# Kernel optimization log

Measured on AMD Instinct MI355X. Metric: run time of the kernel, lower is better.

The kernel has to match this reference:

```python
import jax, jax.numpy as jnp
import numpy as np

N_NODES, D_IN, D_OUT, N_REL, N_EDGES = 100000, 128, 128, 8, 625000


def setup_inputs() -> dict:
    key = jax.random.key(0)
    ks = jax.random.split(key, 6)
    x = jax.random.normal(ks[0], (N_NODES, D_IN), dtype=jnp.float32)
    edge_index = jax.random.randint(ks[1], (2, N_EDGES), 0, N_NODES, dtype=jnp.int64)
    edge_type = jax.random.randint(ks[2], (N_EDGES,), 0, N_REL, dtype=jnp.int64)
    lim = (6.0 / (D_IN + D_OUT)) ** 0.5  # xavier_uniform
    rel_weight = jax.random.uniform(ks[3], (N_REL, D_IN, D_OUT), jnp.float32, -lim, lim)
    self_loop_weight = jax.random.uniform(ks[4], (D_IN, D_OUT), jnp.float32, -lim, lim)
    bias = jnp.zeros((D_OUT,), jnp.float32)
    return dict(x=x, edge_index=edge_index, edge_type=edge_type,
                rel_weight=rel_weight, self_loop_weight=self_loop_weight, bias=bias)


def reference(x, edge_index, edge_type, rel_weight, self_loop_weight, bias):
    N = x.shape[0]
    R = rel_weight.shape[0]
    src, dst = edge_index[0], edge_index[1]
    # Per-(relation, dst) in-degree == torch.bincount(dst) within each relation mask.
    seg = edge_type * N + dst  # combined (rel, dst) segment id
    deg = jax.ops.segment_sum(jnp.ones_like(src, dtype=x.dtype), seg, num_segments=R * N)
    deg = jnp.maximum(deg, 1.0)
    # Transform all node features by each relation weight once: [R, N, Do].
    xW = jnp.einsum('nd,rde->rne', x, rel_weight)
    # Gather per-edge messages already transformed by the edge's relation.
    messages = xW[edge_type, src] / deg[seg][:, None]  # [E, Do]
    out = x @ self_loop_weight + jax.ops.segment_sum(messages, dst, num_segments=N)
    return out + bias
```

## Files before the change

kernel.cpp:

```cpp
#include <hip/hip_runtime.h>

#define N_NODES 100000
#define DIM 128
#define N_REL 8
#define N_EDGES 625000
#define RN 800000
#define N_PADROWS 100032
#define SCAN_BLOCKS 98
#define SCAN_CHUNK 8192

__device__ __forceinline__ unsigned short f2bf(float f) {
    unsigned int u = __float_as_uint(f);
    u += 0x7fffu + ((u >> 16) & 1u);
    return (unsigned short)(u >> 16);
}

__device__ __forceinline__ float bf2f(unsigned short s) {
    return __uint_as_float(((unsigned int)s) << 16);
}

__global__ __launch_bounds__(256) void prep_kernel(const float* __restrict__ x,
                                                   const float* __restrict__ relw,
                                                   const float* __restrict__ selfw,
                                                   const int* __restrict__ dst,
                                                   const int* __restrict__ rel,
                                                   unsigned short* __restrict__ xb,
                                                   unsigned short* __restrict__ Wt,
                                                   int* __restrict__ degi,
                                                   int* __restrict__ rank) {
    int i = blockIdx.x * 256 + threadIdx.x;
    {
        float4 v = *(const float4*)(x + (size_t)i * 4);
        unsigned short t[4] = {f2bf(v.x), f2bf(v.y), f2bf(v.z), f2bf(v.w)};
        *(uint2*)(xb + (size_t)i * 4) = *(const uint2*)t;
    }
    if (i < 512) {
        uint4 z = {0, 0, 0, 0};
        *(uint4*)(xb + (size_t)N_NODES * DIM + i * 8) = z;
    }
    if (i < 147456) {
        int j = i & 7;
        int lane = (i >> 3) & 63;
        int t = (i >> 9) & 7;
        int ks = (i >> 12) & 3;
        int r = i >> 14;
        int m16 = lane & 15, quad = lane >> 4;
        int din = ks * 32 + quad * 8 + j;
        int dout = t * 16 + m16;
        float v = (r < 8) ? relw[(r << 14) + (din << 7) + dout] : selfw[(din << 7) + dout];
        Wt[i] = f2bf(v);
    }
    if (i < N_EDGES) {
        rank[i] = atomicAdd(&degi[rel[i] * N_NODES + dst[i]], 1);
    }
}

__global__ __launch_bounds__(256) void scan_kernel(const int* __restrict__ degi,
                                                   unsigned int* __restrict__ status,
                                                   int* __restrict__ offs) {
    __shared__ int lsum[256];
    __shared__ int lpfx;
    const int tid = threadIdx.x;
    const int b = blockIdx.x;
    const int base = b * SCAN_CHUNK + tid * 32;
    int v[32];
    int s = 0;
#pragma unroll
    for (int j = 0; j < 8; j++) {
        int idx = base + j * 4;
        int4 d = {0, 0, 0, 0};
        if (idx + 3 < RN) d = *(const int4*)(degi + idx);
        else {
            if (idx < RN) d.x = degi[idx];
            if (idx + 1 < RN) d.y = degi[idx + 1];
            if (idx + 2 < RN) d.z = degi[idx + 2];
        }
        v[j * 4] = d.x; v[j * 4 + 1] = d.y; v[j * 4 + 2] = d.z; v[j * 4 + 3] = d.w;
        s += d.x + d.y + d.z + d.w;
    }
    lsum[tid] = s;
    __syncthreads();
    for (int off = 1; off < 256; off <<= 1) {
        int p = (tid >= off) ? lsum[tid - off] : 0;
        __syncthreads();
        lsum[tid] += p;
        __syncthreads();
    }
    int thrbase = lsum[tid] - s;
    int total = lsum[255];

    if (b == 0) {
        if (tid == 0) {
            atomicExch(&status[0], 0x80000000u | (unsigned)total);
            lpfx = 0;
        }
    } else {
        if (tid == 0) atomicExch(&status[b], 0x40000000u | (unsigned)total);
        if (tid < 64) {
            int sum = 0;
            int j = b - 1;
            while (true) {
                int idx = j - tid;
                unsigned st = (idx >= 0) ? atomicAdd(&status[idx], 0u) : 0x80000000u;
                unsigned long long pball = __ballot(st & 0x80000000u);
                unsigned long long zball = __ballot(st == 0u);
                int fp = pball ? (__ffsll(pball) - 1) : 64;
                unsigned long long below = (fp >= 64) ? ~0ull : ((1ull << fp) - 1ull);
                if (zball & below) continue;
                int lim = (fp < 64) ? fp : 63;
                int val = (tid <= lim) ? (int)(st & 0x3fffffffu) : 0;
                for (int o = 32; o > 0; o >>= 1) val += __shfl_down(val, o);
                sum += __shfl(val, 0);
                if (fp < 64) break;
                j -= 64;
            }
            if (tid == 0) {
                atomicExch(&status[b], 0x80000000u | (unsigned)(sum + total));
                lpfx = sum;
            }
        }
    }
    __syncthreads();
    int run = lpfx + thrbase;
#pragma unroll
    for (int j = 0; j < 32; j++) {
        int idx = base + j;
        if (idx < RN) {
            offs[idx] = run;
            if (idx == RN - 1) offs[RN] = run + v[j];
            run += v[j];
        }
    }
}

__global__ __launch_bounds__(256) void fill_kernel(const int* __restrict__ src,
                                                   const int* __restrict__ dst,
                                                   const int* __restrict__ rel,
                                                   const int* __restrict__ rank,
                                                   const int* __restrict__ offs,
                                                   unsigned int* __restrict__ ebuf) {
    int e = blockIdx.x * 256 + threadIdx.x;
    if (e < N_EDGES) {
        int d = dst[e];
        int key = rel[e] * N_NODES + d;
        int pos = offs[key] + rank[e];
        ebuf[pos] = (unsigned int)src[e] | ((unsigned int)(d & 15) << 17);
    }
}

typedef __attribute__((ext_vector_type(8))) short frag8;
typedef __attribute__((ext_vector_type(4))) float f32x4;

__global__ __launch_bounds__(128, 5) void fused_kernel(const unsigned short* __restrict__ xb,
                                                       const unsigned short* __restrict__ Wt,
                                                       const int* __restrict__ offs2,
                                                       const unsigned int* __restrict__ ebuf,
                                                       const float* __restrict__ bias,
                                                       float* __restrict__ out) {
    __shared__ __align__(16) unsigned char ldsraw[8192];

    const int tid = threadIdx.x;
    const int h = tid >> 6, lane = tid & 63;
    const int m16 = lane & 15, quad = lane >> 4;
    const int dbase = blockIdx.x * 16;
    unsigned char* slab = ldsraw + h * 4096;

    int cidx = dbase + lane;
    if (cidx > N_NODES) cidx = N_NODES;
    const int* obase = offs2 + (size_t)h * 4 * N_NODES + cidx;

    int obc = obase[0];
    int obn = obase[N_NODES];

    f32x4 acc[8];
#pragma unroll
    for (int t = 0; t < 8; t++) acc[t] = (f32x4){0.f, 0.f, 0.f, 0.f};

    int s0 = __builtin_amdgcn_readlane(obc, 0);
    int count = __builtin_amdgcn_readlane(obc, 16) - s0;
    unsigned int ewc = 0;
    if (lane < count) ewc = ebuf[s0 + lane];

    {
        const unsigned short* ap = xb + (size_t)(dbase + m16) * DIM;
#pragma unroll
        for (int k2 = 0; k2 < 2; k2++) {
            int ks = h * 2 + k2;
            frag8 a = *(const frag8*)(ap + ks * 32 + quad * 8);
            const frag8* bp = (const frag8*)Wt + ((8 * 4 + ks) * 8) * 64 + lane;
#pragma unroll
            for (int t = 0; t < 8; t++)
                acc[t] = __builtin_amdgcn_mfma_f32_16x16x32_bf16(a, bp[t * 64], acc[t], 0, 0, 0);
        }
    }

    unsigned int u0[8], v0[8];
    if (count > 0) {
        int cl = count; if (cl > 64) cl = 64;
#pragma unroll
        for (int k = 0; k < 8; k++) {
            int li = k; if (li >= cl) li = cl - 1;
            u0[k] = (unsigned int)__builtin_amdgcn_readlane((int)ewc, li);
            v0[k] = *((const unsigned int*)xb + (size_t)(u0[k] & 0x1ffffu) * 64 + lane);
        }
    }

#pragma unroll 1
    for (int r = 0; r < 4; r++) {
        int s0n = __builtin_amdgcn_readlane(obn, 0);
        int cntn = __builtin_amdgcn_readlane(obn, 16) - s0n;
        unsigned int ewn = 0;
        if (r < 3 && lane < cntn) ewn = ebuf[s0n + lane];
        int obn2 = (r < 2) ? obase[(r + 2) * N_NODES] : 0;

        {
            uint4 z = {0, 0, 0, 0};
            *(uint4*)(slab + lane * 16) = z;
            *(uint4*)(slab + 1024 + lane * 16) = z;
            *(uint4*)(slab + 2048 + lane * 16) = z;
            *(uint4*)(slab + 3072 + lane * 16) = z;
        }

        if (count > 0) {
            float ax = 0.f, ay = 0.f;
            int cur = -1, cnt = 0;
#pragma unroll 1
            for (int b0 = 0; b0 < count; b0 += 64) {
                int cl = count - b0; if (cl > 64) cl = 64;
                unsigned int ew = ewc;
                if (b0 > 0) {
                    ew = 0;
                    if (b0 + lane < count) ew = ebuf[s0 + b0 + lane];
#pragma unroll
                    for (int k = 0; k < 8; k++) {
                        int li = k; if (li >= cl) li = cl - 1;
                        u0[k] = (unsigned int)__builtin_amdgcn_readlane((int)ew, li);
                        v0[k] = *((const unsigned int*)xb + (size_t)(u0[k] & 0x1ffffu) * 64 + lane);
                    }
                }
#pragma unroll 1
                for (int i = 0; i < cl; i += 8) {
                    unsigned int u1[8], v1[8];
                    if (i + 8 < cl) {
#pragma unroll
                        for (int k = 0; k < 8; k++) {
                            int li = i + 8 + k; if (li >= cl) li = cl - 1;
                            u1[k] = (unsigned int)__builtin_amdgcn_readlane((int)ew, li);
                            v1[k] = *((const unsigned int*)xb + (size_t)(u1[k] & 0x1ffffu) * 64 + lane);
                        }
                    }
                    int kk = cl - i; if (kk > 8) kk = 8;
#pragma unroll
                    for (int k = 0; k < 8; k++) {
                        if (k < kk) {
                            int dl = (int)((u0[k] >> 17) & 15u);
                            if (dl != cur) {
                                if (cnt > 0) {
                                    float inv = __builtin_amdgcn_rcpf((float)cnt);
                                    unsigned int p = (unsigned int)f2bf(ax * inv) |
                                                     ((unsigned int)f2bf(ay * inv) << 16);
                                    int bb = (lane >> 2) ^ cur;
                                    *(unsigned int*)(slab + cur * 256 + bb * 16 + (lane & 3) * 4) = p;
                                }
                                cur = dl; ax = 0.f; ay = 0.f; cnt = 0;
                            }
                            ax += bf2f((unsigned short)(v0[k] & 0xffffu));
                            ay += bf2f((unsigned short)(v0[k] >> 16));
                            cnt++;
                        }
                    }
                    if (i + 8 < cl) {
#pragma unroll
                        for (int k = 0; k < 8; k++) { u0[k] = u1[k]; v0[k] = v1[k]; }
                    }
                }
            }
            {
                float inv = __builtin_amdgcn_rcpf((float)cnt);
                unsigned int p = (unsigned int)f2bf(ax * inv) |
                                 ((unsigned int)f2bf(ay * inv) << 16);
                int bb = (lane >> 2) ^ cur;
                *(unsigned int*)(slab + cur * 256 + bb * 16 + (lane & 3) * 4) = p;
            }
        }

        if (r < 3 && cntn > 0) {
            int cl = cntn; if (cl > 64) cl = 64;
#pragma unroll
            for (int k = 0; k < 8; k++) {
                int li = k; if (li >= cl) li = cl - 1;
                u0[k] = (unsigned int)__builtin_amdgcn_readlane((int)ewn, li);
                v0[k] = *((const unsigned int*)xb + (size_t)(u0[k] & 0x1ffffu) * 64 + lane);
            }
        }

#pragma unroll
        for (int ks = 0; ks < 4; ks++) {
            int bb = (4 * ks + quad) ^ m16;
            frag8 a = *(const frag8*)(slab + m16 * 256 + bb * 16);
            const frag8* bp = (const frag8*)Wt + (((h * 4 + r) * 4 + ks) * 8) * 64 + lane;
#pragma unroll
            for (int t = 0; t < 8; t++)
                acc[t] = __builtin_amdgcn_mfma_f32_16x16x32_bf16(a, bp[t * 64], acc[t], 0, 0, 0);
        }

        s0 = s0n; count = cntn; ewc = ewn; obn = obn2;
    }

    __syncthreads();
    if (h == 1) {
#pragma unroll
        for (int t = 0; t < 8; t++)
            *(f32x4*)(ldsraw + (t * 64 + lane) * 16) = acc[t];
    }
    __syncthreads();
    if (h == 0) {
#pragma unroll
        for (int t = 0; t < 8; t++) {
            f32x4 m = *(f32x4*)(ldsraw + (t * 64 + lane) * 16);
            acc[t] += m;
        }

        float* S = (float*)ldsraw;
#pragma unroll
        for (int hh = 0; hh < 2; hh++) {
#pragma unroll
            for (int tt = 0; tt < 4; tt++) {
                int t = hh * 4 + tt;
                float bc = bias[t * 16 + m16];
#pragma unroll
                for (int i = 0; i < 4; i++)
                    S[(quad * 4 + i) * 68 + tt * 16 + m16] = acc[t][i] + bc;
            }
#pragma unroll
            for (int c = 0; c < 4; c++) {
                int row16 = c * 4 + quad;
                int gr = dbase + row16;
                if (gr < N_NODES)
                    *(float4*)(out + (size_t)gr * DIM + hh * 64 + m16 * 4) =
                        *(float4*)(S + row16 * 68 + m16 * 4);
            }
        }
    }
}

extern "C" void kernel_launch(void* const* d_in, const int* in_sizes, int n_in,
                              void* d_out, int out_size, void* d_ws, size_t ws_size,
                              hipStream_t stream) {
    const float* x = (const float*)d_in[0];
    const int* edge_index = (const int*)d_in[1];
    const int* edge_type = (const int*)d_in[2];
    const float* relw = (const float*)d_in[3];
    const float* selfw = (const float*)d_in[4];
    const float* bias = (const float*)d_in[5];
    float* out = (float*)d_out;
    (void)in_sizes; (void)n_in; (void)out_size; (void)ws_size;

    char* ws = (char*)d_ws;
    size_t off = 0;
    unsigned short* xb = (unsigned short*)(ws + off); off += (size_t)N_PADROWS * DIM * 2;
    unsigned short* Wt = (unsigned short*)(ws + off); off += (size_t)9 * DIM * DIM * 2;
    int* offs2 = (int*)(ws + off); off += (size_t)(RN + 4) * 4;
    unsigned int* ebuf = (unsigned int*)(ws + off); off += (size_t)N_EDGES * 4;

    int* degi = (int*)d_out;
    unsigned int* status = (unsigned int*)(degi + RN);
    int* rank = (int*)(status + SCAN_BLOCKS + 2);

    const int* src = edge_index;
    const int* dst = edge_index + N_EDGES;

    hipMemsetAsync(degi, 0, (size_t)RN * 4 + (SCAN_BLOCKS + 2) * 4, stream);
    prep_kernel<<<12500, 256, 0, stream>>>(x, relw, selfw, dst, edge_type, xb, Wt, degi, rank);
    scan_kernel<<<SCAN_BLOCKS, 256, 0, stream>>>(degi, status, offs2);
    fill_kernel<<<(N_EDGES + 255) / 256, 256, 0, stream>>>(src, dst, edge_type, rank, offs2, ebuf);
    fused_kernel<<<N_PADROWS / 16, 128, 0, stream>>>(xb, Wt, offs2, ebuf, bias, out);
}
```

Baseline: 278.5 us.

## Split fused RGCN kernel across paired waves sharing aggregated tiles in LDS

The fused kernel moves from 2 waves per 16-node block to 8 waves per 32-node block. Each wave pair aggregates two relations concurrently into separate LDS tiles, and after a barrier each wave multiplies both tiles against half of the output columns (4 accumulators instead of 8). The intent is to halve per-wave serial relation work and accumulator registers, raising parallelism and latency hiding in the gather phase. In exchange it adds block-wide barriers, quadruples LDS use per block, and replaces the LDS-staged float4 output stores with scalar strided stores.

```diff
diff --git a/kernel.cpp b/kernel.cpp
--- a/kernel.cpp
+++ b/kernel.cpp
@@ -151,35 +151,40 @@
 typedef __attribute__((ext_vector_type(8))) short frag8;
 typedef __attribute__((ext_vector_type(4))) float f32x4;
 
-__global__ __launch_bounds__(128, 5) void fused_kernel(const unsigned short* __restrict__ xb,
+__global__ __launch_bounds__(512, 4) void fused_kernel(const unsigned short* __restrict__ xb,
                                                        const unsigned short* __restrict__ Wt,
                                                        const int* __restrict__ offs2,
                                                        const unsigned int* __restrict__ ebuf,
                                                        const float* __restrict__ bias,
                                                        float* __restrict__ out) {
-    __shared__ __align__(16) unsigned char ldsraw[8192];
+    __shared__ __align__(16) unsigned char ldsraw[32768];
 
     const int tid = threadIdx.x;
-    const int h = tid >> 6, lane = tid & 63;
+    const int wave = tid >> 6, lane = tid & 63;
+    const int g = wave >> 2, h = (wave >> 1) & 1, c = wave & 1;
     const int m16 = lane & 15, quad = lane >> 4;
-    const int dbase = blockIdx.x * 16;
-    unsigned char* slab = ldsraw + h * 4096;
+    const int dbase = blockIdx.x * 32 + g * 16;
+    unsigned char* pairT = ldsraw + (g * 2 + h) * 8192;
+    unsigned char* myT = pairT + c * 4096;
+    const unsigned int* xb32 = (const unsigned int*)xb;
 
     int cidx = dbase + lane;
     if (cidx > N_NODES) cidx = N_NODES;
-    const int* obase = offs2 + (size_t)h * 4 * N_NODES + cidx;
-
-    int obc = obase[0];
-    int obn = obase[N_NODES];
-
-    f32x4 acc[8];
-#pragma unroll
-    for (int t = 0; t < 8; t++) acc[t] = (f32x4){0.f, 0.f, 0.f, 0.f};
-
-    int s0 = __builtin_amdgcn_readlane(obc, 0);
-    int count = __builtin_amdgcn_readlane(obc, 16) - s0;
-    unsigned int ewc = 0;
-    if (lane < count) ewc = ebuf[s0 + lane];
+
+    int obA = offs2[(size_t)(h * 4 + c) * N_NODES + cidx];
+    int obB = offs2[(size_t)(h * 4 + c + 2) * N_NODES + cidx];
+
+    f32x4 acc[4];
+#pragma unroll
+    for (int t = 0; t < 4; t++) acc[t] = (f32x4){0.f, 0.f, 0.f, 0.f};
+
+    int sA = __builtin_amdgcn_readlane(obA, 0);
+    int cntA = __builtin_amdgcn_readlane(obA, 16) - sA;
+    int sB = __builtin_amdgcn_readlane(obB, 0);
+    int cntB = __builtin_amdgcn_readlane(obB, 16) - sB;
+    unsigned int ewA = 0, ewB = 0;
+    if (lane < cntA) ewA = ebuf[sA + lane];
+    if (lane < cntB) ewB = ebuf[sB + lane];
 
     {
         const unsigned short* ap = xb + (size_t)(dbase + m16) * DIM;
@@ -187,38 +192,35 @@
         for (int k2 = 0; k2 < 2; k2++) {
             int ks = h * 2 + k2;
             frag8 a = *(const frag8*)(ap + ks * 32 + quad * 8);
-            const frag8* bp = (const frag8*)Wt + ((8 * 4 + ks) * 8) * 64 + lane;
-#pragma unroll
-            for (int t = 0; t < 8; t++)
+            const frag8* bp = (const frag8*)Wt + ((8 * 4 + ks) * 8 + c * 4) * 64 + lane;
+#pragma unroll
+            for (int t = 0; t < 4; t++)
                 acc[t] = __builtin_amdgcn_mfma_f32_16x16x32_bf16(a, bp[t * 64], acc[t], 0, 0, 0);
         }
     }
 
     unsigned int u0[8], v0[8];
-    if (count > 0) {
-        int cl = count; if (cl > 64) cl = 64;
+    if (cntA > 0) {
+        int cl = cntA; if (cl > 64) cl = 64;
 #pragma unroll
         for (int k = 0; k < 8; k++) {
             int li = k; if (li >= cl) li = cl - 1;
-            u0[k] = (unsigned int)__builtin_amdgcn_readlane((int)ewc, li);
-            v0[k] = *((const unsigned int*)xb + (size_t)(u0[k] & 0x1ffffu) * 64 + lane);
-        }
-    }
+            u0[k] = (unsigned int)__builtin_amdgcn_readlane((int)ewA, li);
+            v0[k] = xb32[(size_t)(u0[k] & 0x1ffffu) * 64 + lane];
+        }
+    }
+
+    int s0 = sA, count = cntA;
+    unsigned int ewc = ewA;
 
 #pragma unroll 1
-    for (int r = 0; r < 4; r++) {
-        int s0n = __builtin_amdgcn_readlane(obn, 0);
-        int cntn = __builtin_amdgcn_readlane(obn, 16) - s0n;
-        unsigned int ewn = 0;
-        if (r < 3 && lane < cntn) ewn = ebuf[s0n + lane];
-        int obn2 = (r < 2) ? obase[(r + 2) * N_NODES] : 0;
-
+    for (int it = 0; it < 2; ++it) {
         {
             uint4 z = {0, 0, 0, 0};
-            *(uint4*)(slab + lane * 16) = z;
-            *(uint4*)(slab + 1024 + lane * 16) = z;
-            *(uint4*)(slab + 2048 + lane * 16) = z;
-            *(uint4*)(slab + 3072 + lane * 16) = z;
+            *(uint4*)(myT + lane * 16) = z;
+            *(uint4*)(myT + 1024 + lane * 16) = z;
+            *(uint4*)(myT + 2048 + lane * 16) = z;
+            *(uint4*)(myT + 3072 + lane * 16) = z;
         }
 
         if (count > 0) {
@@ -235,7 +237,7 @@
                     for (int k = 0; k < 8; k++) {
                         int li = k; if (li >= cl) li = cl - 1;
                         u0[k] = (unsigned int)__builtin_amdgcn_readlane((int)ew, li);
-                        v0[k] = *((const unsigned int*)xb + (size_t)(u0[k] & 0x1ffffu) * 64 + lane);
+                        v0[k] = xb32[(size_t)(u0[k] & 0x1ffffu) * 64 + lane];
                     }
                 }
 #pragma unroll 1
@@ -246,7 +248,7 @@
                         for (int k = 0; k < 8; k++) {
                             int li = i + 8 + k; if (li >= cl) li = cl - 1;
                             u1[k] = (unsigned int)__builtin_amdgcn_readlane((int)ew, li);
-                            v1[k] = *((const unsigned int*)xb + (size_t)(u1[k] & 0x1ffffu) * 64 + lane);
+                            v1[k] = xb32[(size_t)(u1[k] & 0x1ffffu) * 64 + lane];
                         }
                     }
                     int kk = cl - i; if (kk > 8) kk = 8;
@@ -260,7 +262,7 @@
                                     unsigned int p = (unsigned int)f2bf(ax * inv) |
                                                      ((unsigned int)f2bf(ay * inv) << 16);
                                     int bb = (lane >> 2) ^ cur;
-                                    *(unsigned int*)(slab + cur * 256 + bb * 16 + (lane & 3) * 4) = p;
+                                    *(unsigned int*)(myT + cur * 256 + bb * 16 + (lane & 3) * 4) = p;
                                 }
                                 cur = dl; ax = 0.f; ay = 0.f; cnt = 0;
                             }
@@ -280,65 +282,63 @@
                 unsigned int p = (unsigned int)f2bf(ax * inv) |
                                  ((unsigned int)f2bf(ay * inv) << 16);
                 int bb = (lane >> 2) ^ cur;
-                *(unsigned int*)(slab + cur * 256 + bb * 16 + (lane & 3) * 4) = p;
-            }
-        }
-
-        if (r < 3 && cntn > 0) {
-            int cl = cntn; if (cl > 64) cl = 64;
+                *(unsigned int*)(myT + cur * 256 + bb * 16 + (lane & 3) * 4) = p;
+            }
+        }
+
+        if (it == 0 && cntB > 0) {
+            int cl = cntB; if (cl > 64) cl = 64;
 #pragma unroll
             for (int k = 0; k < 8; k++) {
                 int li = k; if (li >= cl) li = cl - 1;
-                u0[k] = (unsigned int)__builtin_amdgcn_readlane((int)ewn, li);
-                v0[k] = *((const unsigned int*)xb + (size_t)(u0[k] & 0x1ffffu) * 64 + lane);
-            }
-        }
-
-#pragma unroll
-        for (int ks = 0; ks < 4; ks++) {
-            int bb = (4 * ks + quad) ^ m16;
-            frag8 a = *(const frag8*)(slab + m16 * 256 + bb * 16);
-            const frag8* bp = (const frag8*)Wt + (((h * 4 + r) * 4 + ks) * 8) * 64 + lane;
-#pragma unroll
-            for (int t = 0; t < 8; t++)
-                acc[t] = __builtin_amdgcn_mfma_f32_16x16x32_bf16(a, bp[t * 64], acc[t], 0, 0, 0);
-        }
-
-        s0 = s0n; count = cntn; ewc = ewn; obn = obn2;
-    }
-
-    __syncthreads();
+                u0[k] = (unsigned int)__builtin_amdgcn_readlane((int)ewB, li);
+                v0[k] = xb32[(size_t)(u0[k] & 0x1ffffu) * 64 + lane];
+            }
+        }
+
+        __syncthreads();
+
+#pragma unroll
+        for (int pt = 0; pt < 2; ++pt) {
+            const unsigned char* T = pairT + pt * 4096;
+            int rel = h * 4 + it * 2 + pt;
+#pragma unroll
+            for (int ks = 0; ks < 4; ks++) {
+                int bb = (4 * ks + quad) ^ m16;
+                frag8 a = *(const frag8*)(T + m16 * 256 + bb * 16);
+                const frag8* bp = (const frag8*)Wt + ((rel * 4 + ks) * 8 + c * 4) * 64 + lane;
+#pragma unroll
+                for (int t = 0; t < 4; t++)
+                    acc[t] = __builtin_amdgcn_mfma_f32_16x16x32_bf16(a, bp[t * 64], acc[t], 0, 0, 0);
+            }
+        }
+
+        __syncthreads();
+
+        s0 = sB; count = cntB; ewc = ewB;
+    }
+
+    float* mbuf = (float*)(ldsraw + (g * 2 + c) * 4096);
     if (h == 1) {
 #pragma unroll
-        for (int t = 0; t < 8; t++)
-            *(f32x4*)(ldsraw + (t * 64 + lane) * 16) = acc[t];
+        for (int t = 0; t < 4; t++)
+            *(f32x4*)(mbuf + (t * 64 + lane) * 4) = acc[t];
     }
     __syncthreads();
     if (h == 0) {
 #pragma unroll
-        for (int t = 0; t < 8; t++) {
-            f32x4 m = *(f32x4*)(ldsraw + (t * 64 + lane) * 16);
+        for (int t = 0; t < 4; t++) {
+            f32x4 m = *(f32x4*)(mbuf + (t * 64 + lane) * 4);
             acc[t] += m;
         }
-
-        float* S = (float*)ldsraw;
-#pragma unroll
-        for (int hh = 0; hh < 2; hh++) {
-#pragma unroll
-            for (int tt = 0; tt < 4; tt++) {
-                int t = hh * 4 + tt;
-                float bc = bias[t * 16 + m16];
-#pragma unroll
-                for (int i = 0; i < 4; i++)
-                    S[(quad * 4 + i) * 68 + tt * 16 + m16] = acc[t][i] + bc;
-            }
-#pragma unroll
-            for (int c = 0; c < 4; c++) {
-                int row16 = c * 4 + quad;
-                int gr = dbase + row16;
+#pragma unroll
+        for (int t = 0; t < 4; t++) {
+            float bc = bias[c * 64 + t * 16 + m16];
+#pragma unroll
+            for (int i = 0; i < 4; i++) {
+                int gr = dbase + quad * 4 + i;
                 if (gr < N_NODES)
-                    *(float4*)(out + (size_t)gr * DIM + hh * 64 + m16 * 4) =
-                        *(float4*)(S + row16 * 68 + m16 * 4);
+                    out[(size_t)gr * DIM + c * 64 + t * 16 + m16] = acc[t][i] + bc;
             }
         }
     }
@@ -374,5 +374,5 @@
     prep_kernel<<<12500, 256, 0, stream>>>(x, relw, selfw, dst, edge_type, xb, Wt, degi, rank);
     scan_kernel<<<SCAN_BLOCKS, 256, 0, stream>>>(degi, status, offs2);
     fill_kernel<<<(N_EDGES + 255) / 256, 256, 0, stream>>>(src, dst, edge_type, rank, offs2, ebuf);
-    fused_kernel<<<N_PADROWS / 16, 128, 0, stream>>>(xb, Wt, offs2, ebuf, bias, out);
-}
+    fused_kernel<<<N_PADROWS / 32, 512, 0, stream>>>(xb, Wt, offs2, ebuf, bias, out);
+}
```

Result: no change. 273.6 us (-1.8%).
